# Kernel optimization log

Hardware: AMD Instinct MI355X
Metric: run time of the kernel (lower is better)

## Reference

```python
import jax, jax.numpy as jnp
import numpy as np

N, E, D = 100000, 1600000, 128


def setup_inputs() -> dict:
    key = jax.random.key(0)
    ks = jax.random.split(key, 10)
    x = jax.random.normal(ks[0], (N, D), dtype=jnp.float32)
    edge_index = jax.random.randint(ks[1], (2, E), 0, N, dtype=jnp.int64)
    edge_weight = jax.random.uniform(ks[2], (E,), dtype=jnp.float32)
    s = 1.0 / np.sqrt(D)
    # PyG GraphConv params per layer: lin_rel (weight+bias), lin_root (weight, no bias)
    Wr0 = jax.random.uniform(ks[3], (D, D), jnp.float32, -s, s)
    br0 = jax.random.uniform(ks[4], (D,), jnp.float32, -s, s)
    Ws0 = jax.random.uniform(ks[5], (D, D), jnp.float32, -s, s)
    Wr1 = jax.random.uniform(ks[6], (D, D), jnp.float32, -s, s)
    br1 = jax.random.uniform(ks[7], (D,), jnp.float32, -s, s)
    Ws1 = jax.random.uniform(ks[8], (D, D), jnp.float32, -s, s)
    return {"x": x, "edge_index": edge_index, "edge_weight": edge_weight,
            "Wr0": Wr0, "br0": br0, "Ws0": Ws0,
            "Wr1": Wr1, "br1": br1, "Ws1": Ws1}


def _graph_conv(h, src, dst, Wr, br, Ws, ew=None):
    # message: gather source-node features (optionally scaled by edge weight)
    m = h[src]                                   # [E, D]
    if ew is not None:
        m = m * ew[:, None]
    agg = jax.ops.segment_sum(m, dst, num_segments=h.shape[0])  # [N, D] aggr='add'
    return agg @ Wr + br + h @ Ws                # lin_rel(agg) + lin_root(h)


def reference(x, edge_index, edge_weight, Wr0, br0, Ws0, Wr1, br1, Ws1):
    src, dst = edge_index[0], edge_index[1]
    h = jax.nn.relu(_graph_conv(x, src, dst, Wr0, br0, Ws0, edge_weight))
    h = jax.nn.relu(_graph_conv(h, src, dst, Wr1, br1, Ws1))
    return h
```

## Files before the change

kernel.cpp:

```cpp
#include <hip/hip_runtime.h>
#include <hip/hip_bf16.h>

#ifndef D_FEAT
#define D_FEAT 128
#endif

#define SLOTS 40
#define OVF_CAP 8192

typedef __attribute__((ext_vector_type(8))) short bf16x8;
typedef __attribute__((ext_vector_type(4))) float f32x4;
typedef unsigned long long u64;

__device__ __forceinline__ unsigned short f2bf(float f) {
    union { float f; unsigned u; } v; v.f = f;
    unsigned r = v.u + 0x7FFF + ((v.u >> 16) & 1);
    return (unsigned short)(r >> 16);
}
__device__ __forceinline__ float bf2f_lo(unsigned u) {
    union { unsigned u; float f; } v; v.u = u << 16; return v.f;
}
__device__ __forceinline__ float bf2f_hi(unsigned u) {
    union { unsigned u; float f; } v; v.u = u & 0xFFFF0000u; return v.f;
}

__global__ void scatter_ell(const int* __restrict__ src, const int* __restrict__ dst,
                            const float* __restrict__ ew, int E, int Q, int N,
                            int* __restrict__ pos, unsigned* __restrict__ ell,
                            int* __restrict__ ovf_cnt, int4* __restrict__ ovf) {
    const int p = blockIdx.x & 7;
    const int sub = blockIdx.x >> 3;
    const int nsub = gridDim.x >> 3;
    const int lo = p * Q;
    const int hi = min(lo + Q, N);
    for (int i = sub * 256 + threadIdx.x; i < E; i += nsub * 256) {
        const int d = dst[i];
        if (d >= lo && d < hi) {
            const int slot = atomicAdd(&pos[d], 1);
            if (slot < SLOTS) {
                const unsigned w12 = min(4095u, (unsigned)__float2int_rn(ew[i] * 4095.f));
                ell[(size_t)d * SLOTS + slot] = (unsigned)src[i] | (w12 << 20);
            } else {
                const int o = atomicAdd(ovf_cnt, 1);
                if (o < OVF_CAP)
                    ovf[o] = make_int4(src[i], d, __float_as_int(ew[i]), 0);
            }
        }
    }
}

template <bool WEIGHTED>
__global__ void ovf_fixup(const unsigned short* __restrict__ XH,
                          const int* __restrict__ ovf_cnt,
                          const int4* __restrict__ ovf,
                          unsigned short* __restrict__ AGG) {
    const int n = min(*ovf_cnt, OVF_CAP);
    const int lane = threadIdx.x;
    for (int e = 0; e < n; ++e) {
        const int4 r = ovf[e];
        const float w = WEIGHTED ? __int_as_float(r.z) : 1.f;
        const unsigned u = *reinterpret_cast<const unsigned*>(
            XH + (size_t)(unsigned)r.x * 128 + lane * 2);
        unsigned* pa = reinterpret_cast<unsigned*>(
            AGG + (size_t)r.y * 128 + lane * 2);
        const unsigned cur = *pa;
        const float ax = bf2f_lo(cur) + w * bf2f_lo(u);
        const float ay = bf2f_hi(cur) + w * bf2f_hi(u);
        *pa = (unsigned)f2bf(ax) | ((unsigned)f2bf(ay) << 16);
    }
}

__device__ __forceinline__ void pack_W_body(const float* __restrict__ Wr,
                                            const float* __restrict__ Ws,
                                            unsigned short* __restrict__ Wp,
                                            int t) {
    const int lane = t & 63;
    const int ct = (t >> 6) & 7;
    const int ks = t >> 9;
    const int col = ct * 16 + (lane & 15);
    const int kbase = ks * 32 + (lane >> 4) * 8;
    unsigned short v[8];
#pragma unroll
    for (int j = 0; j < 8; ++j) {
        const int k = kbase + j;
        const float w = (k < 128) ? Wr[(size_t)k * 128 + col]
                                  : Ws[(size_t)(k - 128) * 128 + col];
        v[j] = f2bf(w);
    }
    *reinterpret_cast<uint4*>(Wp + (size_t)t * 8) = *reinterpret_cast<uint4*>(v);
}

__global__ void prep_kernel(const float* __restrict__ x,
                            unsigned short* __restrict__ XH, int N, int nconv,
                            const float* __restrict__ Wr0, const float* __restrict__ Ws0,
                            unsigned short* __restrict__ Wp0,
                            const float* __restrict__ Wr1, const float* __restrict__ Ws1,
                            unsigned short* __restrict__ Wp1) {
    const int b = blockIdx.x;
    if (b < nconv) {
        const int i = b * 256 + threadIdx.x;
        if (i >= N * 32) return;
        float4 v = reinterpret_cast<const float4*>(x)[i];
        unsigned lo = (unsigned)f2bf(v.x) | ((unsigned)f2bf(v.y) << 16);
        unsigned hi = (unsigned)f2bf(v.z) | ((unsigned)f2bf(v.w) << 16);
        reinterpret_cast<uint2*>(XH)[i] = make_uint2(lo, hi);
    } else if (b < nconv + 16) {
        pack_W_body(Wr0, Ws0, Wp0, (b - nconv) * 256 + threadIdx.x);
    } else {
        pack_W_body(Wr1, Ws1, Wp1, (b - nconv - 16) * 256 + threadIdx.x);
    }
}

template <bool WEIGHTED>
__global__ void __launch_bounds__(256)
gather_ell(const unsigned short* __restrict__ XH,
           const int* __restrict__ pos,
           const unsigned* __restrict__ ell,
           unsigned short* __restrict__ AGG,
           int N) {
    const int node = blockIdx.x * 4 + (threadIdx.x >> 6);
    const int lane = threadIdx.x & 63;
    if (node >= N) return;
    const int g = lane >> 4;
    const int c = lane & 15;

    const int deg = min(pos[node], SLOTS);
    const unsigned* ebase = ell + (size_t)node * SLOTS;

    float acc[8];
#pragma unroll
    for (int j = 0; j < 8; ++j) acc[j] = 0.f;

    auto body = [&](int i) {
        const unsigned r = ebase[i];
        const float w = WEIGHTED ? (float)(r >> 20) * (1.f / 4095.f) : 1.f;
        const uint4 v = *reinterpret_cast<const uint4*>(
            XH + (size_t)(r & 0xFFFFF) * 128 + c * 8);
        acc[0] += w * bf2f_lo(v.x); acc[1] += w * bf2f_hi(v.x);
        acc[2] += w * bf2f_lo(v.y); acc[3] += w * bf2f_hi(v.y);
        acc[4] += w * bf2f_lo(v.z); acc[5] += w * bf2f_hi(v.z);
        acc[6] += w * bf2f_lo(v.w); acc[7] += w * bf2f_hi(v.w);
    };

    int i = g;
    for (; i + 12 < deg; i += 16) { body(i); body(i + 4); body(i + 8); body(i + 12); }
    for (; i < deg; i += 4) body(i);

#pragma unroll
    for (int j = 0; j < 8; ++j) {
        acc[j] += __shfl_xor(acc[j], 16);
        acc[j] += __shfl_xor(acc[j], 32);
    }

    if (lane < 16) {
        uint4 o;
        o.x = (unsigned)f2bf(acc[0]) | ((unsigned)f2bf(acc[1]) << 16);
        o.y = (unsigned)f2bf(acc[2]) | ((unsigned)f2bf(acc[3]) << 16);
        o.z = (unsigned)f2bf(acc[4]) | ((unsigned)f2bf(acc[5]) << 16);
        o.w = (unsigned)f2bf(acc[6]) | ((unsigned)f2bf(acc[7]) << 16);
        *reinterpret_cast<uint4*>(AGG + (size_t)node * 128 + c * 8) = o;
    }
}

template <bool TO_BF16>
__global__ void __launch_bounds__(256)
gemm_mfma(const unsigned short* __restrict__ AGG,
          const unsigned short* __restrict__ XH,
          const unsigned short* __restrict__ Wp,
          const float* __restrict__ br,
          float* __restrict__ out,
          unsigned short* __restrict__ XHo,
          int N) {
    const int tid = threadIdx.x;
    const int wave = tid >> 6;
    const int lane = tid & 63;
    const int r0 = blockIdx.x * 128 + wave * 32;
    const int lk = (lane >> 4) * 8;

    int ra = r0 + (lane & 15);
    int rb = ra + 16;
    if (ra >= N) ra = N - 1;
    if (rb >= N) rb = N - 1;
    const unsigned short* paga = AGG + (size_t)ra * 128 + lk;
    const unsigned short* pagb = AGG + (size_t)rb * 128 + lk;
    const unsigned short* pxha = XH + (size_t)ra * 128 + lk;
    const unsigned short* pxhb = XH + (size_t)rb * 128 + lk;
    const unsigned short* pw = Wp + (size_t)lane * 8;

    f32x4 acc[2][8];
#pragma unroll
    for (int rt = 0; rt < 2; ++rt)
#pragma unroll
        for (int ct = 0; ct < 8; ++ct)
            acc[rt][ct] = (f32x4){0.f, 0.f, 0.f, 0.f};

#pragma unroll
    for (int ks = 0; ks < 8; ++ks) {
        const bf16x8 a0 = (ks < 4)
            ? *reinterpret_cast<const bf16x8*>(paga + ks * 32)
            : *reinterpret_cast<const bf16x8*>(pxha + (ks - 4) * 32);
        const bf16x8 a1 = (ks < 4)
            ? *reinterpret_cast<const bf16x8*>(pagb + ks * 32)
            : *reinterpret_cast<const bf16x8*>(pxhb + (ks - 4) * 32);
#pragma unroll
        for (int ct = 0; ct < 8; ++ct) {
            const bf16x8 b = *reinterpret_cast<const bf16x8*>(pw + (((ks << 3) + ct) << 9));
            acc[0][ct] = __builtin_amdgcn_mfma_f32_16x16x32_bf16(a0, b, acc[0][ct], 0, 0, 0);
            acc[1][ct] = __builtin_amdgcn_mfma_f32_16x16x32_bf16(a1, b, acc[1][ct], 0, 0, 0);
        }
    }

    const int crow = (lane >> 4) * 4;
    const int ccol = lane & 15;
#pragma unroll
    for (int ct = 0; ct < 8; ++ct) {
        const int col = ct * 16 + ccol;
        const float bias = br[col];
#pragma unroll
        for (int rt = 0; rt < 2; ++rt) {
#pragma unroll
            for (int reg = 0; reg < 4; ++reg) {
                const int row = r0 + rt * 16 + crow + reg;
                if (row >= N) continue;
                const float v = fmaxf(acc[rt][ct][reg] + bias, 0.f);
                if (TO_BF16) {
                    XHo[(size_t)row * 128 + col] = f2bf(v);
                } else {
                    out[(size_t)row * 128 + col] = v;
                }
            }
        }
    }
}

extern "C" void kernel_launch(void* const* d_in, const int* in_sizes, int n_in,
                              void* d_out, int out_size, void* d_ws, size_t ws_size,
                              hipStream_t stream) {
    const float* x  = (const float*)d_in[0];
    const int*   ei = (const int*)d_in[1];
    const float* ew = (const float*)d_in[2];
    const float* Wr0 = (const float*)d_in[3];
    const float* br0 = (const float*)d_in[4];
    const float* Ws0 = (const float*)d_in[5];
    const float* Wr1 = (const float*)d_in[6];
    const float* br1 = (const float*)d_in[7];
    const float* Ws1 = (const float*)d_in[8];

    const int N = in_sizes[0] / D_FEAT;
    const int E = in_sizes[1] / 2;
    const int* src = ei;
    const int* dst = ei + E;
    const int Q = (N + 7) / 8;

    char* w = (char*)d_ws;
    auto carve = [&](size_t bytes) { char* p = w; w += (bytes + 15) & ~(size_t)15; return p; };
    unsigned short* XH  = (unsigned short*)carve((size_t)N * 128 * 2);
    unsigned short* AGG = (unsigned short*)carve((size_t)N * 128 * 2);
    unsigned short* Wp0 = (unsigned short*)carve(256 * 128 * 2);
    unsigned short* Wp1 = (unsigned short*)carve(256 * 128 * 2);
    int*      pos     = (int*)     carve((size_t)N * 4);
    int*      ovf_cnt = (int*)     carve(16);
    int4*     ovf     = (int4*)    carve((size_t)OVF_CAP * 16);
    unsigned* ell     = (unsigned*)carve((size_t)N * SLOTS * 4);

    float* out = (float*)d_out;

    const int nconv = (N * 32 + 255) / 256;
    const int gather_blocks = (N + 3) / 4;
    const int gemm_blocks = (N + 127) / 128;

    prep_kernel<<<nconv + 32, 256, 0, stream>>>(x, XH, N, nconv,
                                                Wr0, Ws0, Wp0, Wr1, Ws1, Wp1);

    hipMemsetAsync(pos, 0, (size_t)N * 4, stream);
    hipMemsetAsync(ovf_cnt, 0, 4, stream);
    scatter_ell<<<2048, 256, 0, stream>>>(src, dst, ew, E, Q, N, pos, ell, ovf_cnt, ovf);

    gather_ell<true><<<gather_blocks, 256, 0, stream>>>(XH, pos, ell, AGG, N);
    ovf_fixup<true><<<1, 64, 0, stream>>>(XH, ovf_cnt, ovf, AGG);
    gemm_mfma<true><<<gemm_blocks, 256, 0, stream>>>(AGG, XH, Wp0, br0, nullptr, XH, N);

    gather_ell<false><<<gather_blocks, 256, 0, stream>>>(XH, pos, ell, AGG, N);
    ovf_fixup<false><<<1, 64, 0, stream>>>(XH, ovf_cnt, ovf, AGG);
    gemm_mfma<false><<<gemm_blocks, 256, 0, stream>>>(AGG, XH, Wp1, br1, out, nullptr, N);
}
```

Baseline: 293.2 us.

## Fuse prep and ELL scatter into one kernel; drop dst-partitioned scatter passes

Merges the bf16 conversion and weight-packing kernel with the ELL scatter kernel into a single launch, so the conversion blocks can run alongside the scatter blocks. It also removes the 8-way destination-range partitioning of the scatter, so each edge is read once instead of eight times. The cost is that atomics on pos and ELL writes are no longer localized to a node range per block group, which may hurt L2 locality.

```diff
diff --git a/kernel.cpp b/kernel.cpp
--- a/kernel.cpp
+++ b/kernel.cpp
@@ -7,6 +7,7 @@
 
 #define SLOTS 40
 #define OVF_CAP 8192
+#define NSCAT 2048
 
 typedef __attribute__((ext_vector_type(8))) short bf16x8;
 typedef __attribute__((ext_vector_type(4))) float f32x4;
@@ -24,18 +25,41 @@
     union { unsigned u; float f; } v; v.u = u & 0xFFFF0000u; return v.f;
 }
 
-__global__ void scatter_ell(const int* __restrict__ src, const int* __restrict__ dst,
-                            const float* __restrict__ ew, int E, int Q, int N,
-                            int* __restrict__ pos, unsigned* __restrict__ ell,
-                            int* __restrict__ ovf_cnt, int4* __restrict__ ovf) {
-    const int p = blockIdx.x & 7;
-    const int sub = blockIdx.x >> 3;
-    const int nsub = gridDim.x >> 3;
-    const int lo = p * Q;
-    const int hi = min(lo + Q, N);
-    for (int i = sub * 256 + threadIdx.x; i < E; i += nsub * 256) {
-        const int d = dst[i];
-        if (d >= lo && d < hi) {
+__device__ __forceinline__ void pack_W_body(const float* __restrict__ Wr,
+                                            const float* __restrict__ Ws,
+                                            unsigned short* __restrict__ Wp,
+                                            int t) {
+    const int lane = t & 63;
+    const int ct = (t >> 6) & 7;
+    const int ks = t >> 9;
+    const int col = ct * 16 + (lane & 15);
+    const int kbase = ks * 32 + (lane >> 4) * 8;
+    unsigned short v[8];
+#pragma unroll
+    for (int j = 0; j < 8; ++j) {
+        const int k = kbase + j;
+        const float w = (k < 128) ? Wr[(size_t)k * 128 + col]
+                                  : Ws[(size_t)(k - 128) * 128 + col];
+        v[j] = f2bf(w);
+    }
+    *reinterpret_cast<uint4*>(Wp + (size_t)t * 8) = *reinterpret_cast<uint4*>(v);
+}
+
+__global__ void __launch_bounds__(256)
+prep_scatter(const int* __restrict__ src, const int* __restrict__ dst,
+             const float* __restrict__ ew, int E, int N,
+             int* __restrict__ pos, unsigned* __restrict__ ell,
+             int* __restrict__ ovf_cnt, int4* __restrict__ ovf,
+             const float* __restrict__ x, unsigned short* __restrict__ XH,
+             int nconv,
+             const float* __restrict__ Wr0, const float* __restrict__ Ws0,
+             unsigned short* __restrict__ Wp0,
+             const float* __restrict__ Wr1, const float* __restrict__ Ws1,
+             unsigned short* __restrict__ Wp1) {
+    const int b = blockIdx.x;
+    if (b < NSCAT) {
+        for (int i = b * 256 + threadIdx.x; i < E; i += NSCAT * 256) {
+            const int d = dst[i];
             const int slot = atomicAdd(&pos[d], 1);
             if (slot < SLOTS) {
                 const unsigned w12 = min(4095u, (unsigned)__float2int_rn(ew[i] * 4095.f));
@@ -46,6 +70,17 @@
                     ovf[o] = make_int4(src[i], d, __float_as_int(ew[i]), 0);
             }
         }
+    } else if (b < NSCAT + nconv) {
+        const int i = (b - NSCAT) * 256 + threadIdx.x;
+        if (i >= N * 32) return;
+        float4 v = reinterpret_cast<const float4*>(x)[i];
+        unsigned lo = (unsigned)f2bf(v.x) | ((unsigned)f2bf(v.y) << 16);
+        unsigned hi = (unsigned)f2bf(v.z) | ((unsigned)f2bf(v.w) << 16);
+        reinterpret_cast<uint2*>(XH)[i] = make_uint2(lo, hi);
+    } else if (b < NSCAT + nconv + 16) {
+        pack_W_body(Wr0, Ws0, Wp0, (b - NSCAT - nconv) * 256 + threadIdx.x);
+    } else {
+        pack_W_body(Wr1, Ws1, Wp1, (b - NSCAT - nconv - 16) * 256 + threadIdx.x);
     }
 }
 
@@ -70,47 +105,6 @@
     }
 }
 
-__device__ __forceinline__ void pack_W_body(const float* __restrict__ Wr,
-                                            const float* __restrict__ Ws,
-                                            unsigned short* __restrict__ Wp,
-                                            int t) {
-    const int lane = t & 63;
-    const int ct = (t >> 6) & 7;
-    const int ks = t >> 9;
-    const int col = ct * 16 + (lane & 15);
-    const int kbase = ks * 32 + (lane >> 4) * 8;
-    unsigned short v[8];
-#pragma unroll
-    for (int j = 0; j < 8; ++j) {
-        const int k = kbase + j;
-        const float w = (k < 128) ? Wr[(size_t)k * 128 + col]
-                                  : Ws[(size_t)(k - 128) * 128 + col];
-        v[j] = f2bf(w);
-    }
-    *reinterpret_cast<uint4*>(Wp + (size_t)t * 8) = *reinterpret_cast<uint4*>(v);
-}
-
-__global__ void prep_kernel(const float* __restrict__ x,
-                            unsigned short* __restrict__ XH, int N, int nconv,
-                            const float* __restrict__ Wr0, const float* __restrict__ Ws0,
-                            unsigned short* __restrict__ Wp0,
-                            const float* __restrict__ Wr1, const float* __restrict__ Ws1,
-                            unsigned short* __restrict__ Wp1) {
-    const int b = blockIdx.x;
-    if (b < nconv) {
-        const int i = b * 256 + threadIdx.x;
-        if (i >= N * 32) return;
-        float4 v = reinterpret_cast<const float4*>(x)[i];
-        unsigned lo = (unsigned)f2bf(v.x) | ((unsigned)f2bf(v.y) << 16);
-        unsigned hi = (unsigned)f2bf(v.z) | ((unsigned)f2bf(v.w) << 16);
-        reinterpret_cast<uint2*>(XH)[i] = make_uint2(lo, hi);
-    } else if (b < nconv + 16) {
-        pack_W_body(Wr0, Ws0, Wp0, (b - nconv) * 256 + threadIdx.x);
-    } else {
-        pack_W_body(Wr1, Ws1, Wp1, (b - nconv - 16) * 256 + threadIdx.x);
-    }
-}
-
 template <bool WEIGHTED>
 __global__ void __launch_bounds__(256)
 gather_ell(const unsigned short* __restrict__ XH,
@@ -250,7 +244,6 @@
     const int E = in_sizes[1] / 2;
     const int* src = ei;
     const int* dst = ei + E;
-    const int Q = (N + 7) / 8;
 
     char* w = (char*)d_ws;
     auto carve = [&](size_t bytes) { char* p = w; w += (bytes + 15) & ~(size_t)15; return p; };
@@ -269,12 +262,11 @@
     const int gather_blocks = (N + 3) / 4;
     const int gemm_blocks = (N + 127) / 128;
 
-    prep_kernel<<<nconv + 32, 256, 0, stream>>>(x, XH, N, nconv,
-                                                Wr0, Ws0, Wp0, Wr1, Ws1, Wp1);
-
     hipMemsetAsync(pos, 0, (size_t)N * 4, stream);
     hipMemsetAsync(ovf_cnt, 0, 4, stream);
-    scatter_ell<<<2048, 256, 0, stream>>>(src, dst, ew, E, Q, N, pos, ell, ovf_cnt, ovf);
+    prep_scatter<<<NSCAT + nconv + 32, 256, 0, stream>>>(
+        src, dst, ew, E, N, pos, ell, ovf_cnt, ovf,
+        x, XH, nconv, Wr0, Ws0, Wp0, Wr1, Ws1, Wp1);
 
     gather_ell<true><<<gather_blocks, 256, 0, stream>>>(XH, pos, ell, AGG, N);
     ovf_fixup<true><<<1, 64, 0, stream>>>(XH, ovf_cnt, ovf, AGG);
```

New measurement: 326.4 us. 1.11x slower.
